# Performance work log

Hardware: AMD Instinct MI355X
Metric: run time of the kernel (lower is better)

The kernel has to match this reference:

```python
import jax, jax.numpy as jnp
import numpy as np

MU = 5
ITERATIONS = 3


def _sobel(x):
    # torch kernel: stack([K, K.T]) with K = vertical-gradient Sobel; conv2d is cross-correlation
    k = jnp.array([[-1., -2., -1.], [0., 0., 0.], [1., 2., 1.]], dtype=x.dtype)
    kern = jnp.stack([k, k.T])[:, None]  # [2,1,3,3] -> channels (Gy, Gx)
    return jax.lax.conv_general_dilated(
        x, kern, window_strides=(1, 1), padding=[(1, 1), (1, 1)],
        dimension_numbers=("NCHW", "OIHW", "NCHW"))


def _normalize(v):
    # norm over channel dim, zeros replaced by 1 (matches tang_mag[tang_mag==0]=1)
    mag = jnp.linalg.norm(v, axis=1, keepdims=True)
    mag = jnp.where(mag == 0, jnp.ones_like(mag), mag)
    return v / mag


def etf_forward(inputs, mu=MU, iterations=ITERATIONS):
    B, _, H, W = inputs.shape
    sobel = _sobel(inputs)                                   # [B,2,H,W]
    sobel_mag = jnp.linalg.norm(sobel, axis=1, keepdims=True)
    sobel_mag = sobel_mag / jnp.max(sobel_mag)               # [B,1,H,W]
    pad = lambda t: jnp.pad(t, ((0, 0), (0, 0), (mu, mu), (mu, mu)))
    sobel_mag_padded = pad(sobel_mag)
    sobel_X = sobel_mag
    # tang = sobel.flip(channels) * [-1, 1] => [-Gx, Gy], then normalized
    tang = jnp.stack([-sobel[:, 1], sobel[:, 0]], axis=1)
    tang = _normalize(tang)
    for _ in range(iterations):
        for ori in ("Vertical", "Horizontal"):
            tang_padded = pad(tang)
            tang_X = tang
            acc = jnp.zeros_like(tang)
            for i in range(2 * mu + 1):
                if ori == "Vertical":
                    tang_Y = tang_padded[:, :, i:i + H, mu:mu + W]
                    sobel_Y = sobel_mag_padded[:, :, i:i + H, mu:mu + W]
                else:
                    tang_Y = tang_padded[:, :, mu:mu + H, i:i + W]
                    sobel_Y = sobel_mag_padded[:, :, mu:mu + H, i:i + W]
                w = (jnp.tanh(sobel_Y - sobel_X) + 1.0) * jnp.sum(tang_X * tang_Y, axis=1, keepdims=True) * 0.5
                acc = acc + tang_Y * w
            tang = _normalize(acc)
    return tang


def setup_inputs() -> dict:
    key = jax.random.key(0)
    inputs = jax.random.uniform(key, (2, 1, 1024, 1024), dtype=jnp.float32)
    return {"inputs": inputs}


def reference(inputs) -> jnp.ndarray:
    return etf_forward(inputs)
```

## Files before the change

kernel.cpp:

```cpp
#include <hip/hip_runtime.h>

#define BB 2
#define HH 1024
#define WW 1024
#define MU 5

__device__ __forceinline__ float fast_rcp(float x) { return __builtin_amdgcn_rcpf(x); }
__device__ __forceinline__ float fast_rsq(float x) { return __builtin_amdgcn_rsqf(x); }

#define SR 8
__global__ __launch_bounds__(256) void sobel_init(
    const float* __restrict__ x,
    float2* __restrict__ tf,
    float* __restrict__ mag,
    float* __restrict__ block_max)
{
    __shared__ float xs[SR + 2][264];
    const int t = threadIdx.x;
    const int w0 = blockIdx.x * 256;
    const int h0 = blockIdx.y * SR;
    const int b = blockIdx.z;
    const size_t plane = (size_t)HH * WW;
    const float* xb = x + (size_t)b * plane;

    for (int i = t; i < (SR + 2) * 66; i += 256) {
        int r = i / 66, c4 = i % 66;
        int g = h0 - 1 + r;
        int gw = w0 - 4 + 4 * c4;
        float4 v = make_float4(0.f, 0.f, 0.f, 0.f);
        if (g >= 0 && g < HH && gw >= 0 && gw < WW)
            v = *(const float4*)(xb + (size_t)g * WW + gw);
        *(float4*)&xs[r][4 * c4] = v;
    }
    __syncthreads();

    float lmax = 0.f;
    const int c = 4 + t;
    #pragma unroll
    for (int k = 0; k < SR; ++k) {
        const float* rT = xs[k], * rM = xs[k + 1], * rB = xs[k + 2];
        float tl = rT[c - 1], tc = rT[c], tr = rT[c + 1];
        float ml = rM[c - 1],             mr = rM[c + 1];
        float bl = rB[c - 1], bc = rB[c], br = rB[c + 1];
        float s0 = (bl - tl) + 2.f * (bc - tc) + (br - tr);
        float s1 = (tr - tl) + 2.f * (mr - ml) + (br - bl);
        float m = sqrtf(fmaf(s0, s0, s1 * s1));
        float inv = (m == 0.f) ? 1.f : fast_rcp(m);
        size_t gi = (size_t)(h0 + k) * WW + (w0 + t);
        mag[(size_t)b * plane + gi] = m;
        tf[(size_t)b * plane + gi] = make_float2(-s1 * inv, s0 * inv);
        lmax = fmaxf(lmax, m);
    }

    #pragma unroll
    for (int off = 32; off; off >>= 1) lmax = fmaxf(lmax, __shfl_down(lmax, off, 64));
    __shared__ float smax[4];
    if ((t & 63) == 0) smax[t >> 6] = lmax;
    __syncthreads();
    if (t == 0)
        block_max[(blockIdx.z * 128 + blockIdx.y) * 4 + blockIdx.x] =
            fmaxf(fmaxf(smax[0], smax[1]), fmaxf(smax[2], smax[3]));
}

__global__ __launch_bounds__(256) void reduce_max(
    const float* __restrict__ block_max, float* __restrict__ gmax)
{
    const int t = threadIdx.x;
    float m = 0.f;
    #pragma unroll
    for (int i = 0; i < 4; ++i) m = fmaxf(m, block_max[t + 256 * i]);
    #pragma unroll
    for (int off = 32; off; off >>= 1) m = fmaxf(m, __shfl_down(m, off, 64));
    __shared__ float smax[4];
    if ((t & 63) == 0) smax[t >> 6] = m;
    __syncthreads();
    if (t == 0) gmax[0] = fmaxf(fmaxf(smax[0], smax[1]), fmaxf(smax[2], smax[3]));
}

__global__ __launch_bounds__(256) void mag2em(
    float* __restrict__ mag, const float* __restrict__ gmax)
{
    const float s = 2.f * fast_rcp(gmax[0]);
    const int i = blockIdx.x * 256 + threadIdx.x;
    float4* p = (float4*)mag + i;
    float4 v = *p;
    v.x = __expf(-s * v.x);
    v.y = __expf(-s * v.y);
    v.z = __expf(-s * v.z);
    v.w = __expf(-s * v.w);
    *p = v;
}

#define VSTRIP 8
__global__ __launch_bounds__(256) void etf_v(
    const float2* __restrict__ tin, float2* __restrict__ tout,
    const float* __restrict__ em)
{
    const int c  = blockIdx.x * 256 + threadIdx.x;
    const int r0 = blockIdx.y * VSTRIP;
    const int b  = blockIdx.z;
    const size_t plane = (size_t)HH * WW;
    const float2* tb = tin + (size_t)b * plane;
    const float*  eb = em  + (size_t)b * plane;

    float w0[VSTRIP + 10], w1[VSTRIP + 10], we[VSTRIP + 10];
    #pragma unroll
    for (int j = 0; j < 10; ++j) {
        int g = r0 - MU + j;
        float2 v = make_float2(0.f, 0.f); float e = 1.f;
        if (g >= 0) { v = tb[(size_t)g * WW + c]; e = eb[(size_t)g * WW + c]; }
        w0[j] = v.x; w1[j] = v.y; we[j] = e;
    }
    #pragma unroll
    for (int i = 0; i < VSTRIP; ++i) {
        int g = r0 + i + MU;
        float2 v = make_float2(0.f, 0.f); float e = 1.f;
        if (g < HH) { v = tb[(size_t)g * WW + c]; e = eb[(size_t)g * WW + c]; }
        w0[i + 10] = v.x; w1[i + 10] = v.y; we[i + 10] = e;

        float tx0 = w0[i + MU], tx1 = w1[i + MU];
        float remx = fast_rcp(we[i + MU]);
        float a0 = 0.f, a1 = 0.f;
        #pragma unroll
        for (int d = 0; d <= 2 * MU; ++d) {
            float s = fast_rcp(fmaf(we[i + d], remx, 1.f));
            float w = s * fmaf(tx0, w0[i + d], tx1 * w1[i + d]);
            a0 = fmaf(w0[i + d], w, a0);
            a1 = fmaf(w1[i + d], w, a1);
        }
        float n2 = fmaf(a0, a0, a1 * a1);
        float inv = (n2 == 0.f) ? 1.f : fast_rsq(n2);
        tout[(size_t)b * plane + (size_t)(r0 + i) * WW + c] = make_float2(a0 * inv, a1 * inv);
    }
}

template <int PLANAR_OUT>
__global__ __launch_bounds__(256) void etf_h(
    const float2* __restrict__ tin, float* __restrict__ tout,
    const float* __restrict__ em)
{
    __shared__ float2 sT[32][81];
    __shared__ float  sE[32][83];
    const int t = threadIdx.x;
    const int w0 = blockIdx.x * 64;
    const int h0 = blockIdx.y * 32;
    const int b = blockIdx.z;
    const size_t plane = (size_t)HH * WW;
    const float2* tb = tin + (size_t)b * plane;
    const float*  eb = em  + (size_t)b * plane;

    for (int i = t; i < 1920; i += 256) {
        if (i < 1280) {
            int r = i / 40, c4 = i % 40;
            int gw = w0 - 8 + 2 * c4;
            float4 v = make_float4(0.f, 0.f, 0.f, 0.f);
            if (gw >= 0 && gw < WW)
                v = *(const float4*)(tb + (size_t)(h0 + r) * WW + gw);
            sT[r][c4 * 2]     = make_float2(v.x, v.y);
            sT[r][c4 * 2 + 1] = make_float2(v.z, v.w);
        } else {
            int j = i - 1280;
            int r = j / 20, c4 = j % 20;
            int gw = w0 - 8 + 4 * c4;
            float4 v = make_float4(1.f, 1.f, 1.f, 1.f);
            if (gw >= 0 && gw < WW)
                v = *(const float4*)(eb + (size_t)(h0 + r) * WW + gw);
            sE[r][4 * c4] = v.x; sE[r][4 * c4 + 1] = v.y;
            sE[r][4 * c4 + 2] = v.z; sE[r][4 * c4 + 3] = v.w;
        }
    }
    __syncthreads();

    const int r  = t & 31;
    const int cg = t >> 5;
    const int cb = 8 + cg * 8;
    float h0a[18], h1a[18], hea[18];
    #pragma unroll
    for (int j = 0; j < 18; ++j) {
        float2 v = sT[r][cb - MU + j];
        h0a[j] = v.x; h1a[j] = v.y;
        hea[j] = sE[r][cb - MU + j];
    }

    #pragma unroll
    for (int k = 0; k < 8; ++k) {
        float tx0 = h0a[k + MU], tx1 = h1a[k + MU];
        float remx = fast_rcp(hea[k + MU]);
        float a0 = 0.f, a1 = 0.f;
        #pragma unroll
        for (int d = 0; d <= 2 * MU; ++d) {
            float s = fast_rcp(fmaf(hea[k + d], remx, 1.f));
            float w = s * fmaf(tx0, h0a[k + d], tx1 * h1a[k + d]);
            a0 = fmaf(h0a[k + d], w, a0);
            a1 = fmaf(h1a[k + d], w, a1);
        }
        float n2 = fmaf(a0, a0, a1 * a1);
        float inv = (n2 == 0.f) ? 1.f : fast_rsq(n2);
        size_t gi = (size_t)(h0 + r) * WW + (w0 + cg * 8 + k);
        if (PLANAR_OUT) {
            tout[(size_t)(2 * b)     * plane + gi] = a0 * inv;
            tout[(size_t)(2 * b + 1) * plane + gi] = a1 * inv;
        } else {
            ((float2*)tout)[(size_t)b * plane + gi] = make_float2(a0 * inv, a1 * inv);
        }
    }
}

extern "C" void kernel_launch(void* const* d_in, const int* in_sizes, int n_in,
                              void* d_out, int out_size, void* d_ws, size_t ws_size,
                              hipStream_t stream)
{
    const float* x = (const float*)d_in[0];
    char* ws = (char*)d_ws;
    const size_t plane = (size_t)HH * WW;

    float2* tfA = (float2*)ws;
    float2* tfB = (float2*)(ws + sizeof(float) * BB * 2 * plane);
    float* mag  = (float*)(ws + sizeof(float) * BB * 4 * plane);
    float* gmax = (float*)(ws + sizeof(float) * BB * 6 * plane);
    float* block_max = gmax + 16;

    sobel_init<<<dim3(4, 128, BB), 256, 0, stream>>>(x, tfA, mag, block_max);
    reduce_max<<<1, 256, 0, stream>>>(block_max, gmax);
    mag2em<<<dim3(BB * plane / 1024), 256, 0, stream>>>(mag, gmax);

    dim3 gv(4, HH / VSTRIP, BB);
    dim3 gh(WW / 64, HH / 32, BB);
    etf_v<<<gv, 256, 0, stream>>>(tfA, tfB, mag);
    etf_h<0><<<gh, 256, 0, stream>>>(tfB, (float*)tfA, mag);
    etf_v<<<gv, 256, 0, stream>>>(tfA, tfB, mag);
    etf_h<0><<<gh, 256, 0, stream>>>(tfB, (float*)tfA, mag);
    etf_v<<<gv, 256, 0, stream>>>(tfA, tfB, mag);
    etf_h<1><<<gh, 256, 0, stream>>>(tfB, (float*)d_out, mag);
}
```

Measured before the change: 152.2 us.

## Fuse max reduction and exp transform into ETF passes, stage etf_h output in LDS

Measured after the change: 153.6 us. Within noise of the previous version (+0.9%).

```diff
diff --git a/kernel.cpp b/kernel.cpp
--- a/kernel.cpp
+++ b/kernel.cpp
@@ -4,6 +4,7 @@
 #define HH 1024
 #define WW 1024
 #define MU 5
+#define VSTRIP 8
 
 __device__ __forceinline__ float fast_rcp(float x) { return __builtin_amdgcn_rcpf(x); }
 __device__ __forceinline__ float fast_rsq(float x) { return __builtin_amdgcn_rsqf(x); }
@@ -62,71 +63,58 @@
             fmaxf(fmaxf(smax[0], smax[1]), fmaxf(smax[2], smax[3]));
 }
 
-__global__ __launch_bounds__(256) void reduce_max(
-    const float* __restrict__ block_max, float* __restrict__ gmax)
-{
-    const int t = threadIdx.x;
-    float m = 0.f;
-    #pragma unroll
-    for (int i = 0; i < 4; ++i) m = fmaxf(m, block_max[t + 256 * i]);
+__device__ __forceinline__ float gmax_prologue(const float* __restrict__ block_max,
+                                               int t, float* smax)
+{
+    float m = fmaxf(fmaxf(block_max[t], block_max[t + 256]),
+                    fmaxf(block_max[t + 512], block_max[t + 768]));
     #pragma unroll
     for (int off = 32; off; off >>= 1) m = fmaxf(m, __shfl_down(m, off, 64));
-    __shared__ float smax[4];
     if ((t & 63) == 0) smax[t >> 6] = m;
     __syncthreads();
-    if (t == 0) gmax[0] = fmaxf(fmaxf(smax[0], smax[1]), fmaxf(smax[2], smax[3]));
-}
-
-__global__ __launch_bounds__(256) void mag2em(
-    float* __restrict__ mag, const float* __restrict__ gmax)
-{
-    const float s = 2.f * fast_rcp(gmax[0]);
-    const int i = blockIdx.x * 256 + threadIdx.x;
-    float4* p = (float4*)mag + i;
-    float4 v = *p;
-    v.x = __expf(-s * v.x);
-    v.y = __expf(-s * v.y);
-    v.z = __expf(-s * v.z);
-    v.w = __expf(-s * v.w);
-    *p = v;
-}
-
-#define VSTRIP 8
+    float gm = fmaxf(fmaxf(smax[0], smax[1]), fmaxf(smax[2], smax[3]));
+    return 2.f * fast_rcp(gm);
+}
+
 __global__ __launch_bounds__(256) void etf_v(
     const float2* __restrict__ tin, float2* __restrict__ tout,
-    const float* __restrict__ em)
-{
-    const int c  = blockIdx.x * 256 + threadIdx.x;
+    const float* __restrict__ mag, const float* __restrict__ block_max)
+{
+    __shared__ float smax[4];
+    const int t = threadIdx.x;
+    const float s2 = gmax_prologue(block_max, t, smax);
+
+    const int c  = blockIdx.x * 256 + t;
     const int r0 = blockIdx.y * VSTRIP;
     const int b  = blockIdx.z;
     const size_t plane = (size_t)HH * WW;
     const float2* tb = tin + (size_t)b * plane;
-    const float*  eb = em  + (size_t)b * plane;
-
-    float w0[VSTRIP + 10], w1[VSTRIP + 10], we[VSTRIP + 10];
+    const float*  mb = mag + (size_t)b * plane;
+
+    float w0a[VSTRIP + 10], w1a[VSTRIP + 10], wea[VSTRIP + 10];
     #pragma unroll
     for (int j = 0; j < 10; ++j) {
         int g = r0 - MU + j;
-        float2 v = make_float2(0.f, 0.f); float e = 1.f;
-        if (g >= 0) { v = tb[(size_t)g * WW + c]; e = eb[(size_t)g * WW + c]; }
-        w0[j] = v.x; w1[j] = v.y; we[j] = e;
+        float2 v = make_float2(0.f, 0.f); float mr = 0.f;
+        if (g >= 0) { v = tb[(size_t)g * WW + c]; mr = mb[(size_t)g * WW + c]; }
+        w0a[j] = v.x; w1a[j] = v.y; wea[j] = __expf(-s2 * mr);
     }
     #pragma unroll
     for (int i = 0; i < VSTRIP; ++i) {
         int g = r0 + i + MU;
-        float2 v = make_float2(0.f, 0.f); float e = 1.f;
-        if (g < HH) { v = tb[(size_t)g * WW + c]; e = eb[(size_t)g * WW + c]; }
-        w0[i + 10] = v.x; w1[i + 10] = v.y; we[i + 10] = e;
-
-        float tx0 = w0[i + MU], tx1 = w1[i + MU];
-        float remx = fast_rcp(we[i + MU]);
+        float2 v = make_float2(0.f, 0.f); float mr = 0.f;
+        if (g < HH) { v = tb[(size_t)g * WW + c]; mr = mb[(size_t)g * WW + c]; }
+        w0a[i + 10] = v.x; w1a[i + 10] = v.y; wea[i + 10] = __expf(-s2 * mr);
+
+        float tx0 = w0a[i + MU], tx1 = w1a[i + MU];
+        float remx = fast_rcp(wea[i + MU]);
         float a0 = 0.f, a1 = 0.f;
         #pragma unroll
         for (int d = 0; d <= 2 * MU; ++d) {
-            float s = fast_rcp(fmaf(we[i + d], remx, 1.f));
-            float w = s * fmaf(tx0, w0[i + d], tx1 * w1[i + d]);
-            a0 = fmaf(w0[i + d], w, a0);
-            a1 = fmaf(w1[i + d], w, a1);
+            float s = fast_rcp(fmaf(wea[i + d], remx, 1.f));
+            float w = s * fmaf(tx0, w0a[i + d], tx1 * w1a[i + d]);
+            a0 = fmaf(w0a[i + d], w, a0);
+            a1 = fmaf(w1a[i + d], w, a1);
         }
         float n2 = fmaf(a0, a0, a1 * a1);
         float inv = (n2 == 0.f) ? 1.f : fast_rsq(n2);
@@ -137,17 +125,24 @@
 template <int PLANAR_OUT>
 __global__ __launch_bounds__(256) void etf_h(
     const float2* __restrict__ tin, float* __restrict__ tout,
-    const float* __restrict__ em)
-{
-    __shared__ float2 sT[32][81];
-    __shared__ float  sE[32][83];
+    const float* __restrict__ mag, const float* __restrict__ block_max)
+{
+    __shared__ __align__(16) char smem[31360];
+    __shared__ float smax[4];
+    float2 (*sT)[81] = (float2(*)[81])smem;
+    float* sE  = (float*)(smem + 20736);
+    float* sv0 = (float*)smem;
+    float* sv1 = (float*)smem + 32 * 81;
+
     const int t = threadIdx.x;
+    const float s2 = gmax_prologue(block_max, t, smax);
+
     const int w0 = blockIdx.x * 64;
     const int h0 = blockIdx.y * 32;
     const int b = blockIdx.z;
     const size_t plane = (size_t)HH * WW;
     const float2* tb = tin + (size_t)b * plane;
-    const float*  eb = em  + (size_t)b * plane;
+    const float*  mb = mag + (size_t)b * plane;
 
     for (int i = t; i < 1920; i += 256) {
         if (i < 1280) {
@@ -162,11 +157,14 @@
             int j = i - 1280;
             int r = j / 20, c4 = j % 20;
             int gw = w0 - 8 + 4 * c4;
-            float4 v = make_float4(1.f, 1.f, 1.f, 1.f);
+            float4 v = make_float4(0.f, 0.f, 0.f, 0.f);
             if (gw >= 0 && gw < WW)
-                v = *(const float4*)(eb + (size_t)(h0 + r) * WW + gw);
-            sE[r][4 * c4] = v.x; sE[r][4 * c4 + 1] = v.y;
-            sE[r][4 * c4 + 2] = v.z; sE[r][4 * c4 + 3] = v.w;
+                v = *(const float4*)(mb + (size_t)(h0 + r) * WW + gw);
+            float* dst = &sE[r * 83 + 4 * c4];
+            dst[0] = __expf(-s2 * v.x);
+            dst[1] = __expf(-s2 * v.y);
+            dst[2] = __expf(-s2 * v.z);
+            dst[3] = __expf(-s2 * v.w);
         }
     }
     __syncthreads();
@@ -179,8 +177,9 @@
     for (int j = 0; j < 18; ++j) {
         float2 v = sT[r][cb - MU + j];
         h0a[j] = v.x; h1a[j] = v.y;
-        hea[j] = sE[r][cb - MU + j];
-    }
+        hea[j] = sE[r * 83 + cb - MU + j];
+    }
+    __syncthreads();
 
     #pragma unroll
     for (int k = 0; k < 8; ++k) {
@@ -196,12 +195,23 @@
         }
         float n2 = fmaf(a0, a0, a1 * a1);
         float inv = (n2 == 0.f) ? 1.f : fast_rsq(n2);
-        size_t gi = (size_t)(h0 + r) * WW + (w0 + cg * 8 + k);
+        sv0[r * 81 + cb + k] = a0 * inv;
+        sv1[r * 81 + cb + k] = a1 * inv;
+    }
+    __syncthreads();
+
+    #pragma unroll
+    for (int m = 0; m < 8; ++m) {
+        int px = t + 256 * m;
+        int rr = px >> 6, cc = px & 63;
+        float v0 = sv0[rr * 81 + 8 + cc];
+        float v1 = sv1[rr * 81 + 8 + cc];
+        size_t gi = (size_t)(h0 + rr) * WW + (w0 + cc);
         if (PLANAR_OUT) {
-            tout[(size_t)(2 * b)     * plane + gi] = a0 * inv;
-            tout[(size_t)(2 * b + 1) * plane + gi] = a1 * inv;
+            tout[(size_t)(2 * b)     * plane + gi] = v0;
+            tout[(size_t)(2 * b + 1) * plane + gi] = v1;
         } else {
-            ((float2*)tout)[(size_t)b * plane + gi] = make_float2(a0 * inv, a1 * inv);
+            ((float2*)tout)[(size_t)b * plane + gi] = make_float2(v0, v1);
         }
     }
 }
@@ -217,19 +227,16 @@
     float2* tfA = (float2*)ws;
     float2* tfB = (float2*)(ws + sizeof(float) * BB * 2 * plane);
     float* mag  = (float*)(ws + sizeof(float) * BB * 4 * plane);
-    float* gmax = (float*)(ws + sizeof(float) * BB * 6 * plane);
-    float* block_max = gmax + 16;
+    float* block_max = (float*)(ws + sizeof(float) * BB * 5 * plane);
 
     sobel_init<<<dim3(4, 128, BB), 256, 0, stream>>>(x, tfA, mag, block_max);
-    reduce_max<<<1, 256, 0, stream>>>(block_max, gmax);
-    mag2em<<<dim3(BB * plane / 1024), 256, 0, stream>>>(mag, gmax);
 
     dim3 gv(4, HH / VSTRIP, BB);
     dim3 gh(WW / 64, HH / 32, BB);
-    etf_v<<<gv, 256, 0, stream>>>(tfA, tfB, mag);
-    etf_h<0><<<gh, 256, 0, stream>>>(tfB, (float*)tfA, mag);
-    etf_v<<<gv, 256, 0, stream>>>(tfA, tfB, mag);
-    etf_h<0><<<gh, 256, 0, stream>>>(tfB, (float*)tfA, mag);
-    etf_v<<<gv, 256, 0, stream>>>(tfA, tfB, mag);
-    etf_h<1><<<gh, 256, 0, stream>>>(tfB, (float*)d_out, mag);
-}
+    etf_v<<<gv, 256, 0, stream>>>(tfA, tfB, mag, block_max);
+    etf_h<0><<<gh, 256, 0, stream>>>(tfB, (float*)tfA, mag, block_max);
+    etf_v<<<gv, 256, 0, stream>>>(tfA, tfB, mag, block_max);
+    etf_h<0><<<gh, 256, 0, stream>>>(tfB, (float*)tfA, mag, block_max);
+    etf_v<<<gv, 256, 0, stream>>>(tfA, tfB, mag, block_max);
+    etf_h<1><<<gh, 256, 0, stream>>>(tfB, (float*)d_out, mag, block_max);
+}
```
